# Performance work log

Measured on AMD Instinct MI355X. Metric: run time of the kernel, lower is better.

The kernel has to match this reference:

```python
import jax, jax.numpy as jnp
import numpy as np

B, LQ, LK, D = 32, 512, 1024, 128   # batch, query times, key times, channels
E, H, NH = 128, 8, 512               # embed_time, heads, nhidden
DK = E // H


def setup_inputs() -> dict:
    key = jax.random.key(0)
    ks = jax.random.split(key, 9)
    return {
        "query": jax.random.uniform(ks[0], (B, LQ), dtype=jnp.float32),
        "key": jax.random.uniform(ks[1], (B, LK), dtype=jnp.float32),
        "value": jax.random.normal(ks[2], (B, LK, D), dtype=jnp.float32),
        "mask": jax.random.randint(ks[3], (B, LK, D), 0, 2).astype(jnp.int32),
        # TimeEmbedding periodic: Linear(1, E) -> weight [E], bias [E]
        "w_t": jax.random.normal(ks[4], (E,), dtype=jnp.float32) * (1.0 / np.sqrt(1.0)),
        "b_t": jax.random.normal(ks[5], (E,), dtype=jnp.float32) * 0.02,
        # linears[0], linears[1]: Linear(E, E, bias=False), torch layout [out, in]
        "W0": jax.random.normal(ks[6], (E, E), dtype=jnp.float32) * (1.0 / np.sqrt(E)),
        "W1": jax.random.normal(ks[7], (E, E), dtype=jnp.float32) * (1.0 / np.sqrt(E)),
        # linears[2]: Linear(H*D, NH, bias=False)
        "W2": jax.random.normal(ks[8], (NH, H * D), dtype=jnp.float32) * (1.0 / np.sqrt(H * D)),
    }


def reference(query, key, value, mask, w_t, b_t, W0, W1, W2):
    b, lk, d = value.shape
    # periodic time embedding: sin(w*t + b)  -> [B, L, E]
    q_emb = jnp.sin(query[..., None] * w_t + b_t)
    k_emb = jnp.sin(key[..., None] * w_t + b_t)
    # project and split heads -> [B, H, L, DK]
    q = (q_emb @ W0.T).reshape(b, -1, H, DK).transpose(0, 2, 1, 3)
    k = (k_emb @ W1.T).reshape(b, -1, H, DK).transpose(0, 2, 1, 3)
    scores = jnp.einsum("bhqe,bhke->bhqk", q, k) / float(np.sqrt(DK))  # [B,H,LQ,LK]
    # per-channel masked softmax over keys, expressed without the 5D blow-up:
    # p[b,h,q,k,d] = mask[b,k,d]*e[b,h,q,k] / sum_k' mask[b,k',d]*e[b,h,q,k']
    e = jnp.exp(scores - jnp.max(scores, axis=-1, keepdims=True))
    mv = mask.astype(value.dtype)  # [B,LK,D]
    num = jnp.einsum("bhqk,bkd->bhqd", e, mv * value)
    den = jnp.einsum("bhqk,bkd->bhqd", e, mv)
    x = num / den  # [B,H,LQ,D]
    x = x.transpose(0, 2, 1, 3).reshape(b, -1, H * d)  # [B,LQ,H*D]
    return x @ W2.T  # [B,LQ,NH]
```

## Files before the change

kernel.cpp:

```cpp
#include <hip/hip_runtime.h>
#include <math.h>


typedef _Float16 f16;
typedef _Float16 half8 __attribute__((ext_vector_type(8)));
typedef _Float16 half4 __attribute__((ext_vector_type(4)));
typedef float f32x4 __attribute__((ext_vector_type(4)));

#define MFMA_16x16x32_F16(a, b, c) __builtin_amdgcn_mfma_f32_16x16x32_f16((a), (b), (c), 0, 0, 0)

__global__ __launch_bounds__(256, 2)
void embed_project_mfma(const float* __restrict__ times_q,
                        const float* __restrict__ times_k,
                        const float* __restrict__ W0,
                        const float* __restrict__ W1,
                        const float* __restrict__ wt,
                        const float* __restrict__ bt,
                        f16* __restrict__ q_out,
                        f16* __restrict__ k_out) {
    const int bid = blockIdx.x;
    const bool is_q = bid < 128;
    const float* times = is_q ? times_q : times_k;
    const float* W = is_q ? W0 : W1;
    f16* outp = is_q ? q_out : k_out;
    const int r0 = (is_q ? bid : bid - 128) * 128;

    __shared__ f16 w_lds[128][136];
    __shared__ float wv[128];
    __shared__ float bvv[128];
    __shared__ float tv_s[128];

    const int t = threadIdx.x;
    if (t < 128) { wv[t] = wt[t]; bvv[t] = bt[t]; tv_s[t] = times[r0 + t]; }
#pragma unroll
    for (int p = 0; p < 16; ++p) {
        const int idx = p * 256 + t;
        const int row = idx >> 5, c4 = idx & 31;
        float4 v = *(const float4*)(W + (size_t)row * 128 + c4 * 4);
        half4 o = { (f16)v.x, (f16)v.y, (f16)v.z, (f16)v.w };
        *(half4*)&w_lds[row][c4 * 4] = o;
    }
    __syncthreads();

    const int lane = t & 63, wid = t >> 6;
    const int r = wid >> 1, c = wid & 1, l15 = lane & 15, g = lane >> 4;
    f32x4 acc[4][4];
    {
        f32x4 z4 = {};
#pragma unroll
        for (int i = 0; i < 4; ++i)
#pragma unroll
            for (int j = 0; j < 4; ++j) acc[i][j] = z4;
    }
#pragma unroll
    for (int ks = 0; ks < 4; ++ks) {
        half8 bf[4];
#pragma unroll
        for (int nt = 0; nt < 4; ++nt)
            bf[nt] = *(const half8*)&w_lds[c * 64 + nt * 16 + l15][ks * 32 + g * 8];
#pragma unroll
        for (int mt = 0; mt < 4; ++mt) {
            const float tvv = tv_s[r * 64 + mt * 16 + l15];
            half8 ahi, alo;
#pragma unroll
            for (int i = 0; i < 8; ++i) {
                const int j = ks * 32 + g * 8 + i;
                const float s = sinf(tvv * wv[j] + bvv[j]);
                const f16 hi = (f16)s;
                ahi[i] = hi;
                alo[i] = (f16)(s - (float)hi);
            }
#pragma unroll
            for (int nt = 0; nt < 4; ++nt) {
                acc[mt][nt] = MFMA_16x16x32_F16(ahi, bf[nt], acc[mt][nt]);
                acc[mt][nt] = MFMA_16x16x32_F16(alo, bf[nt], acc[mt][nt]);
            }
        }
    }
#pragma unroll
    for (int i = 0; i < 4; ++i)
#pragma unroll
        for (int j = 0; j < 4; ++j)
#pragma unroll
            for (int rr = 0; rr < 4; ++rr) {
                const int row = r0 + r * 64 + i * 16 + g * 4 + rr;
                const int e = c * 64 + j * 16 + l15;
                outp[(size_t)row * 128 + e] = (f16)acc[i][j][rr];
            }
}

__global__ __launch_bounds__(256)
void make_bnbdT(const float* __restrict__ value, const int* __restrict__ mask,
                f16* __restrict__ bnbdT) {
    const int b = blockIdx.x >> 4;
    const int k0 = (blockIdx.x & 15) * 64;
    const int t = threadIdx.x;
    __shared__ f16 bnT[128][72];
    __shared__ f16 bdT[128][72];
    const int d4 = (t & 31) * 4, kk0 = t >> 5;
#pragma unroll
    for (int pass = 0; pass < 8; ++pass) {
        const int kk = pass * 8 + kk0;
        const size_t off = ((size_t)(b * 1024 + k0 + kk)) * 128 + d4;
        float4 vv = *(const float4*)(value + off);
        int4 mm = *(const int4*)(mask + off);
        bnT[d4 + 0][kk] = (f16)(mm.x ? vv.x : 0.f);  bdT[d4 + 0][kk] = (f16)(mm.x ? 1.f : 0.f);
        bnT[d4 + 1][kk] = (f16)(mm.y ? vv.y : 0.f);  bdT[d4 + 1][kk] = (f16)(mm.y ? 1.f : 0.f);
        bnT[d4 + 2][kk] = (f16)(mm.z ? vv.z : 0.f);  bdT[d4 + 2][kk] = (f16)(mm.z ? 1.f : 0.f);
        bnT[d4 + 3][kk] = (f16)(mm.w ? vv.w : 0.f);  bdT[d4 + 3][kk] = (f16)(mm.w ? 1.f : 0.f);
    }
    __syncthreads();
    const int kkb = t & 7, nr = t >> 3;
#pragma unroll
    for (int pass = 0; pass < 8; ++pass) {
        const int n = pass * 32 + nr;
        half8 v = (n < 128) ? *(const half8*)&bnT[n][kkb * 8]
                            : *(const half8*)&bdT[n - 128][kkb * 8];
        *(half8*)(bnbdT + ((size_t)(b * 256 + n)) * 1024 + k0 + kkb * 8) = v;
    }
}

__global__ void cvt_f16(const float* __restrict__ in, f16* __restrict__ out) {
    const int i = blockIdx.x * 256 + threadIdx.x;
    float4 v = ((const float4*)in)[i];
    half4 o = { (f16)v.x, (f16)v.y, (f16)v.z, (f16)v.w };
    ((half4*)out)[i] = o;
}

__global__ __launch_bounds__(256, 2)
void fused_attn_mfma(const f16* __restrict__ q_s,
                     const f16* __restrict__ k_s,
                     const f16* __restrict__ bnbdT,
                     f16* __restrict__ x16) {
    const int bid = blockIdx.x;
    const int qt = bid & 3, h = (bid >> 2) & 7, b = bid >> 5;
    const int q0 = qt * 128;
    const int t = threadIdx.x, lane = t & 63, wid = t >> 6;
    const int r = wid >> 1, c = wid & 1;
    const int l15 = lane & 15, g = lane >> 4;

    __shared__ f16 k_t[64][40];
    __shared__ f16 e_t[128][72];
    __shared__ f16 bv_t[256][72];

    half8 zero8 = {};
    for (int i = t; i < 64 * 40 / 8; i += 256) ((half8*)k_t)[i] = zero8;

    half8 qa[4];
    {
        const f16* qbase = q_s + ((size_t)(b * 512 + q0 + r * 64)) * 128 + h * 16 + g * 8;
#pragma unroll
        for (int mt = 0; mt < 4; ++mt) {
            half8 v = zero8;
            if (g < 2) v = *(const half8*)(qbase + (size_t)(mt * 16 + l15) * 128);
            qa[mt] = v;
        }
    }

    f32x4 acc[4][8];
    {
        f32x4 z4 = {};
#pragma unroll
        for (int i = 0; i < 4; ++i)
#pragma unroll
            for (int j = 0; j < 8; ++j) acc[i][j] = z4;
    }

    const f16* kbase = k_s + ((size_t)b * 1024) * 128 + h * 16;
    const f16* bvbase = bnbdT + ((size_t)b * 256) * 1024;
    const int kkb = t & 7, nr = t >> 3;

    for (int kc = 0; kc < 16; ++kc) {
        const int k0 = kc * 64;
        __syncthreads();
        if (t < 128) {
            const int kk = t >> 1, jh = t & 1;
            *(half8*)&k_t[kk][jh * 8] = *(const half8*)(kbase + (size_t)(k0 + kk) * 128 + jh * 8);
        }
#pragma unroll
        for (int pass = 0; pass < 8; ++pass) {
            const int n = pass * 32 + nr;
            *(half8*)&bv_t[n][kkb * 8] =
                *(const half8*)(bvbase + (size_t)n * 1024 + k0 + kkb * 8);
        }
        __syncthreads();
#pragma unroll
        for (int kt = 0; kt < 2; ++kt) {
            half8 kb = *(const half8*)&k_t[c * 32 + kt * 16 + l15][g * 8];
            f32x4 s[4];
#pragma unroll
            for (int mt = 0; mt < 4; ++mt) {
                f32x4 z = {};
                s[mt] = MFMA_16x16x32_F16(kb, qa[mt], z);
            }
#pragma unroll
            for (int mt = 0; mt < 4; ++mt) {
                half4 ev;
#pragma unroll
                for (int rr = 0; rr < 4; ++rr)
                    ev[rr] = (f16)__expf(s[mt][rr] * 0.25f);
                *(half4*)&e_t[r * 64 + mt * 16 + l15][c * 32 + kt * 16 + g * 4] = ev;
            }
        }
        __syncthreads();
#pragma unroll
        for (int ks = 0; ks < 2; ++ks) {
            half8 af[4];
#pragma unroll
            for (int mt = 0; mt < 4; ++mt)
                af[mt] = *(const half8*)&e_t[r * 64 + mt * 16 + l15][ks * 32 + g * 8];
#pragma unroll
            for (int nt = 0; nt < 8; ++nt) {
                const int n = (nt < 4) ? (c * 64 + nt * 16 + l15)
                                       : (128 + c * 64 + (nt - 4) * 16 + l15);
                half8 bf = *(const half8*)&bv_t[n][ks * 32 + g * 8];
#pragma unroll
                for (int mt = 0; mt < 4; ++mt)
                    acc[mt][nt] = MFMA_16x16x32_F16(af[mt], bf, acc[mt][nt]);
            }
        }
    }
#pragma unroll
    for (int mt = 0; mt < 4; ++mt) {
#pragma unroll
        for (int nt = 0; nt < 4; ++nt) {
#pragma unroll
            for (int rr = 0; rr < 4; ++rr) {
                const int q = q0 + r * 64 + mt * 16 + g * 4 + rr;
                const int d = c * 64 + nt * 16 + l15;
                const float xv = acc[mt][nt][rr] / acc[mt][nt + 4][rr];
                x16[((size_t)(b * 512 + q)) * 1024 + h * 128 + d] = (f16)xv;
            }
        }
    }
}

__global__ __launch_bounds__(256, 2)
void out_gemm_f16(const f16* __restrict__ x16, const f16* __restrict__ w2,
                  float* __restrict__ outp) {
    const int bid = blockIdx.x;
    const int m0 = (bid >> 2) * 128, n0 = (bid & 3) * 128;
    const int t = threadIdx.x, lane = t & 63, wid = t >> 6;
    const int r = wid >> 1, c = wid & 1, l15 = lane & 15, g = lane >> 4;
    __shared__ f16 a_t[128][72];
    __shared__ f16 b_t[128][72];
    f32x4 acc[4][4];
    {
        f32x4 z4 = {};
#pragma unroll
        for (int i = 0; i < 4; ++i)
#pragma unroll
            for (int j = 0; j < 4; ++j) acc[i][j] = z4;
    }
    const int kkb = t & 7, nr = t >> 3;
    for (int kc = 0; kc < 16; ++kc) {
        const int k0 = kc * 64;
        __syncthreads();
#pragma unroll
        for (int pass = 0; pass < 4; ++pass) {
            const int row = pass * 32 + nr;
            *(half8*)&a_t[row][kkb * 8] =
                *(const half8*)(x16 + (size_t)(m0 + row) * 1024 + k0 + kkb * 8);
            *(half8*)&b_t[row][kkb * 8] =
                *(const half8*)(w2 + (size_t)(n0 + row) * 1024 + k0 + kkb * 8);
        }
        __syncthreads();
#pragma unroll
        for (int ks = 0; ks < 2; ++ks) {
            half8 af[4], bf[4];
#pragma unroll
            for (int i = 0; i < 4; ++i) {
                af[i] = *(const half8*)&a_t[r * 64 + i * 16 + l15][ks * 32 + g * 8];
                bf[i] = *(const half8*)&b_t[c * 64 + i * 16 + l15][ks * 32 + g * 8];
            }
#pragma unroll
            for (int i = 0; i < 4; ++i)
#pragma unroll
                for (int j = 0; j < 4; ++j)
                    acc[i][j] = MFMA_16x16x32_F16(af[i], bf[j], acc[i][j]);
        }
    }
#pragma unroll
    for (int i = 0; i < 4; ++i)
#pragma unroll
        for (int j = 0; j < 4; ++j)
#pragma unroll
            for (int rr = 0; rr < 4; ++rr) {
                const int m = m0 + r * 64 + i * 16 + g * 4 + rr;
                const int n = n0 + c * 64 + j * 16 + l15;
                outp[(size_t)m * 512 + n] = acc[i][j][rr];
            }
}

extern "C" void kernel_launch(void* const* d_in, const int* in_sizes, int n_in,
                              void* d_out, int out_size, void* d_ws, size_t ws_size,
                              hipStream_t stream) {
    const float* query = (const float*)d_in[0];
    const float* key   = (const float*)d_in[1];
    const float* value = (const float*)d_in[2];
    const int*   mask  = (const int*)d_in[3];
    const float* w_t   = (const float*)d_in[4];
    const float* b_t   = (const float*)d_in[5];
    const float* W0    = (const float*)d_in[6];
    const float* W1    = (const float*)d_in[7];
    const float* W2    = (const float*)d_in[8];
    float* outp = (float*)d_out;

    f16* wsh = (f16*)d_ws;
    f16* q_s16  = wsh;
    f16* k_s16  = q_s16 + (size_t)2097152;
    f16* bnbdT  = k_s16 + (size_t)4194304;
    f16* x16    = bnbdT + (size_t)8388608;
    f16* w2_16  = x16 + (size_t)16777216;

    embed_project_mfma<<<384, 256, 0, stream>>>(query, key, W0, W1, w_t, b_t,
                                                q_s16, k_s16);
    make_bnbdT<<<512, 256, 0, stream>>>(value, mask, bnbdT);
    cvt_f16<<<512, 256, 0, stream>>>(W2, w2_16);
    fused_attn_mfma<<<1024, 256, 0, stream>>>(q_s16, k_s16, bnbdT, x16);
    out_gemm_f16<<<512, 256, 0, stream>>>(x16, w2_16, outp);
}
```

Measured before the change: 263.9 us.

## Prefetch global tiles into registers and remap attention block order

In the attention kernel, the next K-chunk's key and value/mask tiles are loaded from global memory into registers while the current chunk is being computed, so memory latency overlaps with MFMA work. The output GEMM gets the same treatment with two register buffers, loading two chunks ahead. The attention block index is also remapped so that consecutive blocks handle different batches, which changes L2 locality and how work spreads across the device. The cost is many more live registers (8 or 16 half8 vectors per thread), which could lower occupancy under launch_bounds(256,2) or cause spills.

After: 234.6 us. 1.12x faster.

```diff
diff --git a/kernel.cpp b/kernel.cpp
--- a/kernel.cpp
+++ b/kernel.cpp
@@ -132,8 +132,10 @@
                      const f16* __restrict__ k_s,
                      const f16* __restrict__ bnbdT,
                      f16* __restrict__ x16) {
-    const int bid = blockIdx.x;
-    const int qt = bid & 3, h = (bid >> 2) & 7, b = bid >> 5;
+    const int p = blockIdx.x;
+    const int b = (p & 7) + ((p >> 8) << 3);
+    const int hq = (p >> 3) & 31;
+    const int h = hq >> 2, qt = hq & 3;
     const int q0 = qt * 128;
     const int t = threadIdx.x, lane = t & 63, wid = t >> 6;
     const int r = wid >> 1, c = wid & 1;
@@ -170,20 +172,32 @@
     const f16* bvbase = bnbdT + ((size_t)b * 256) * 1024;
     const int kkb = t & 7, nr = t >> 3;
 
+    half8 bv_reg[8];
+    half8 k_reg;
+
+#define FA_LOAD_CHUNK(K0)                                                          \
+    do {                                                                           \
+        if (t < 128)                                                               \
+            k_reg = *(const half8*)(kbase + (size_t)((K0) + (t >> 1)) * 128 +      \
+                                    (t & 1) * 8);                                  \
+        _Pragma("unroll")                                                          \
+        for (int pass = 0; pass < 8; ++pass)                                       \
+            bv_reg[pass] = *(const half8*)(bvbase + (size_t)(pass * 32 + nr) *     \
+                                           1024 + (K0) + kkb * 8);                 \
+    } while (0)
+
+    FA_LOAD_CHUNK(0);
+
     for (int kc = 0; kc < 16; ++kc) {
-        const int k0 = kc * 64;
-        __syncthreads();
-        if (t < 128) {
-            const int kk = t >> 1, jh = t & 1;
-            *(half8*)&k_t[kk][jh * 8] = *(const half8*)(kbase + (size_t)(k0 + kk) * 128 + jh * 8);
-        }
-#pragma unroll
-        for (int pass = 0; pass < 8; ++pass) {
-            const int n = pass * 32 + nr;
-            *(half8*)&bv_t[n][kkb * 8] =
-                *(const half8*)(bvbase + (size_t)n * 1024 + k0 + kkb * 8);
-        }
-        __syncthreads();
+        __syncthreads();
+        if (t < 128)
+            *(half8*)&k_t[t >> 1][(t & 1) * 8] = k_reg;
+#pragma unroll
+        for (int pass = 0; pass < 8; ++pass)
+            *(half8*)&bv_t[pass * 32 + nr][kkb * 8] = bv_reg[pass];
+        __syncthreads();
+        if (kc < 15) FA_LOAD_CHUNK((kc + 1) * 64);
+
 #pragma unroll
         for (int kt = 0; kt < 2; ++kt) {
             half8 kb = *(const half8*)&k_t[c * 32 + kt * 16 + l15][g * 8];
@@ -220,6 +234,8 @@
             }
         }
     }
+#undef FA_LOAD_CHUNK
+
 #pragma unroll
     for (int mt = 0; mt < 4; ++mt) {
 #pragma unroll
@@ -253,18 +269,34 @@
             for (int j = 0; j < 4; ++j) acc[i][j] = z4;
     }
     const int kkb = t & 7, nr = t >> 3;
+
+    half8 a_reg[2][4], b_reg[2][4];
+#define OG_LOAD(BUF, K0)                                                           \
+    do {                                                                           \
+        _Pragma("unroll")                                                          \
+        for (int pass = 0; pass < 4; ++pass) {                                     \
+            const int row = pass * 32 + nr;                                        \
+            a_reg[BUF][pass] = *(const half8*)(x16 + (size_t)(m0 + row) * 1024 +   \
+                                               (K0) + kkb * 8);                    \
+            b_reg[BUF][pass] = *(const half8*)(w2 + (size_t)(n0 + row) * 1024 +    \
+                                               (K0) + kkb * 8);                    \
+        }                                                                          \
+    } while (0)
+
+    OG_LOAD(0, 0);
+    OG_LOAD(1, 64);
+
     for (int kc = 0; kc < 16; ++kc) {
-        const int k0 = kc * 64;
+        const int cur = kc & 1;
         __syncthreads();
 #pragma unroll
         for (int pass = 0; pass < 4; ++pass) {
             const int row = pass * 32 + nr;
-            *(half8*)&a_t[row][kkb * 8] =
-                *(const half8*)(x16 + (size_t)(m0 + row) * 1024 + k0 + kkb * 8);
-            *(half8*)&b_t[row][kkb * 8] =
-                *(const half8*)(w2 + (size_t)(n0 + row) * 1024 + k0 + kkb * 8);
-        }
-        __syncthreads();
+            *(half8*)&a_t[row][kkb * 8] = a_reg[cur][pass];
+            *(half8*)&b_t[row][kkb * 8] = b_reg[cur][pass];
+        }
+        __syncthreads();
+        if (kc + 2 < 16) OG_LOAD(cur, (kc + 2) * 64);
 #pragma unroll
         for (int ks = 0; ks < 2; ++ks) {
             half8 af[4], bf[4];
@@ -280,6 +312,8 @@
                     acc[i][j] = MFMA_16x16x32_F16(af[i], bf[j], acc[i][j]);
         }
     }
+#undef OG_LOAD
+
 #pragma unroll
     for (int i = 0; i < 4; ++i)
 #pragma unroll
```
